# Kernel tuning notes

Hardware: AMD Instinct MI355X
Metric: run time of the kernel (lower is better)

The kernel has to match this reference:

```python
import jax, jax.numpy as jnp
import numpy as np

B, C, RES, WS, HEADS, GROUPS, MLP_DIM = 16, 256, 56, 7, 8, 16, 1024
HEAD_DIM = C // HEADS
N = WS * WS  # tokens per window


def _rel_index(ws):
    coords = np.stack(np.meshgrid(np.arange(ws), np.arange(ws), indexing='ij'), 0).reshape(2, -1)
    rel = (coords[:, :, None] - coords[:, None, :]).transpose(1, 2, 0) + ws - 1
    return jnp.asarray(rel[..., 0] * (2 * ws - 1) + rel[..., 1], jnp.int32)


def setup_inputs() -> dict:
    key = jax.random.key(0)
    ks = jax.random.split(key, 8)
    s = 0.02
    return {
        'x': jax.random.normal(ks[0], (B, C, RES, RES), jnp.float32),
        'qkv_w': jax.random.normal(ks[1], (3 * C, C), jnp.float32) * s,
        'qkv_b': jnp.zeros((3 * C,), jnp.float32),
        'logit_scale': jnp.full((HEADS,), np.log(10.0), jnp.float32),
        'bias_table': jax.random.normal(ks[2], ((2 * WS - 1) ** 2, HEADS), jnp.float32) * s,
        'rel_index': _rel_index(WS),
        'proj_w': jax.random.normal(ks[3], (C, C), jnp.float32) * s,
        'proj_b': jnp.zeros((C,), jnp.float32),
        'gn1_w': jnp.ones((C,), jnp.float32), 'gn1_b': jnp.zeros((C,), jnp.float32),
        'gn2_w': jnp.ones((C,), jnp.float32), 'gn2_b': jnp.zeros((C,), jnp.float32),
        'mlp_gn_w': jnp.ones((C,), jnp.float32), 'mlp_gn_b': jnp.zeros((C,), jnp.float32),
        'mlp_w1': jax.random.normal(ks[4], (MLP_DIM, C), jnp.float32) * s,
        'mlp_b1': jnp.zeros((MLP_DIM,), jnp.float32),
        'mlp_w2': jax.random.normal(ks[5], (C, MLP_DIM), jnp.float32) * s,
        'mlp_b2': jnp.zeros((C,), jnp.float32),
    }


def _group_norm(x, w, b, groups, eps=1e-5):
    bn, c, h, ww = x.shape
    xg = x.reshape(bn, groups, c // groups, h, ww)
    m = xg.mean((2, 3, 4), keepdims=True)
    v = xg.var((2, 3, 4), keepdims=True)
    xg = (xg - m) * jax.lax.rsqrt(v + eps)
    return xg.reshape(bn, c, h, ww) * w[None, :, None, None] + b[None, :, None, None]


def _window_cosine_attn(x, qkv_w, qkv_b, logit_scale, bias_table, rel_index, proj_w, proj_b):
    bn, c, hh, ww = x.shape
    nh, nw = hh // WS, ww // WS
    # partition into non-overlapping WSxWS windows -> [bn*nh*nw, N, C]
    xw = x.reshape(bn, c, nh, WS, nw, WS).transpose(0, 2, 4, 3, 5, 1).reshape(bn * nh * nw, N, c)
    qkv = xw @ qkv_w.T + qkv_b
    qkv = qkv.reshape(-1, N, 3, HEADS, HEAD_DIM).transpose(2, 0, 3, 1, 4)
    q, k, v = qkv[0], qkv[1], qkv[2]  # [Bw, heads, N, d]
    # cosine attention (Swin v2): l2-normalized q/k, learnable clamped logit scale
    qn = q / jnp.clip(jnp.linalg.norm(q, axis=-1, keepdims=True), 1e-12)
    kn = k / jnp.clip(jnp.linalg.norm(k, axis=-1, keepdims=True), 1e-12)
    scale = jnp.exp(jnp.minimum(logit_scale, jnp.log(100.0)))[None, :, None, None]
    attn = jnp.einsum('bhnd,bhmd->bhnm', qn, kn) * scale
    bias = bias_table[rel_index].transpose(2, 0, 1)  # [heads, N, N]
    attn = jax.nn.softmax(attn + bias[None], axis=-1)
    out = jnp.einsum('bhnm,bhmd->bhnd', attn, v)
    out = out.transpose(0, 2, 1, 3).reshape(-1, N, c) @ proj_w.T + proj_b
    # reverse window partition -> [bn, c, H, W]
    out = out.reshape(bn, nh, nw, WS, WS, c).transpose(0, 5, 1, 3, 2, 4).reshape(bn, c, hh, ww)
    return out


def reference(x, qkv_w, qkv_b, logit_scale, bias_table, rel_index, proj_w, proj_b,
              gn1_w, gn1_b, gn2_w, gn2_b, mlp_gn_w, mlp_gn_b, mlp_w1, mlp_b1, mlp_w2, mlp_b2):
    h = _window_cosine_attn(x, qkv_w, qkv_b, logit_scale, bias_table, rel_index, proj_w, proj_b)
    h = jax.nn.relu(_group_norm(x + h, gn1_w, gn1_b, GROUPS))
    # ConvMLP: GroupNorm -> 1x1 conv -> act -> 1x1 conv
    m = _group_norm(h, mlp_gn_w, mlp_gn_b, GROUPS)
    m = jax.nn.relu(jnp.einsum('bchw,ec->behw', m, mlp_w1) + mlp_b1[None, :, None, None])
    m = jnp.einsum('behw,ce->bchw', m, mlp_w2) + mlp_b2[None, :, None, None]
    z = jax.nn.relu(_group_norm(h + m, gn2_w, gn2_b, GROUPS))
    return z
```

## Files before the change

kernel.cpp:

```cpp
#include <hip/hip_runtime.h>
#include <hip/hip_bf16.h>

typedef unsigned short u16;
typedef u16 u16x8 __attribute__((ext_vector_type(8)));
typedef u16 u16x4 __attribute__((ext_vector_type(4)));
typedef __bf16 bf16x8 __attribute__((ext_vector_type(8)));
typedef float f32x4 __attribute__((ext_vector_type(4)));

#define B_      16
#define C_      256
#define RES_    56
#define HW_     3136
#define NTOK    49
#define HEADS_  8
#define HD_     32
#define GROUPS_ 16
#define MLPD    1024
#define M_TOT   50176

__device__ __forceinline__ float b2f(u16 u){
  unsigned int x = ((unsigned int)u) << 16;
  return __builtin_bit_cast(float, x);
}
__device__ __forceinline__ u16 f2b(float f){
  __hip_bfloat16 h = __float2bfloat16(f);
  return __builtin_bit_cast(u16, h);
}
__device__ __forceinline__ bool sniff_f32(const void* sniff){
  return ((const u16*)sniff)[0] != (u16)0x3F80;
}
__device__ __forceinline__ float ldf(const void* p, size_t i, bool f32){
  return f32 ? ((const float*)p)[i] : b2f(((const u16*)p)[i]);
}
__device__ __forceinline__ void load8(const void* p, size_t off, bool f32, float* v){
  if (f32){
    const float* s = (const float*)p + off;
    float4 a = *(const float4*)s, b = *(const float4*)(s + 4);
    v[0]=a.x; v[1]=a.y; v[2]=a.z; v[3]=a.w; v[4]=b.x; v[5]=b.y; v[6]=b.z; v[7]=b.w;
  } else {
    u16x8 u = *(const u16x8*)((const u16*)p + off);
    #pragma unroll
    for (int j=0;j<8;++j) v[j] = b2f(u[j]);
  }
}

__device__ __forceinline__ void gload16(const u16* g, u16* l){
  __builtin_amdgcn_global_load_lds(
      (const __attribute__((address_space(1))) unsigned int*)g,
      (__attribute__((address_space(3))) unsigned int*)l, 16, 0, 0);
}

__device__ __forceinline__ int tok_of(int base_hw, int i){
  int ic = i < 48 ? i : 48;
  int q = (ic*37) >> 8;
  return base_hw + q*RES_ + (ic - q*7);
}

enum { M_QKV=0, M_PROJ=1, M_MLP1=2, M_MLP2=3 };

template<int MODE>
__global__ __launch_bounds__(256)
void mgemm(const u16* __restrict__ A, const u16* __restrict__ Bseg,
           const void* __restrict__ bias, void* __restrict__ Cp,
           const void* __restrict__ resid, float2* __restrict__ partE,
           const void* __restrict__ sniff)
{
  constexpr int KK = (MODE==M_MLP2) ? 1024 : 256;
  constexpr bool STATS = (MODE==M_PROJ || MODE==M_MLP2);
  const int nx  = gridDim.x;
  const int bid = blockIdx.y * nx + blockIdx.x;
  const int cpx = (nx * gridDim.y) >> 3;
  const int swz = (bid & 7) * cpx + (bid >> 3);
  const int n0 = (swz % nx) * 128;
  const int m0 = (swz / nx) * 128;

  __shared__ alignas(16) u16 As[128*64];
  __shared__ alignas(16) u16 Bs[128*64];
  __shared__ float pS[4][2][4], pQ[4][2][4];
  const int tid  = threadIdx.x;
  const int lane = tid & 63, w = tid >> 6;
  const int wm = w >> 1, wn = w & 1;
  const int lr = lane & 15, lk = lane >> 4;

  const int grow = lane >> 3, gcolg = (lane & 7) ^ (lane >> 3);
  size_t aoff[4], boff[4];
  #pragma unroll
  for (int i=0;i<4;++i){
    const int row = w*32 + i*8 + grow;
    aoff[i] = (size_t)(m0 + row)*KK + gcolg*8;
    boff[i] = (size_t)(n0 + row)*KK + gcolg*8;
  }

  f32x4 acc[4][4];
  #pragma unroll
  for (int i=0;i<4;++i)
    #pragma unroll
    for (int j=0;j<4;++j) acc[i][j] = (f32x4){0.f,0.f,0.f,0.f};

  for (int k0 = 0; k0 < KK; k0 += 64){
    if (k0) __syncthreads();
    #pragma unroll
    for (int i=0;i<4;++i){
      gload16(A    + aoff[i] + k0, As + (w*4+i)*512);
      gload16(Bseg + boff[i] + k0, Bs + (w*4+i)*512);
    }
    __syncthreads();
    #pragma unroll
    for (int kh=0; kh<2; ++kh){
      bf16x8 af[4], bfr[4];
      #pragma unroll
      for (int mf=0;mf<4;++mf){
        int row = wm*64 + mf*16 + lr;
        int idx = (row*64 + (kh*4 + lk)*8) ^ ((row&7)*8);
        af[mf] = *(const bf16x8*)(As + idx);
      }
      #pragma unroll
      for (int nf=0;nf<4;++nf){
        int row = wn*64 + nf*16 + lr;
        int idx = (row*64 + (kh*4 + lk)*8) ^ ((row&7)*8);
        bfr[nf] = *(const bf16x8*)(Bs + idx);
      }
      #pragma unroll
      for (int mf=0;mf<4;++mf)
        #pragma unroll
        for (int nf=0;nf<4;++nf)
          acc[mf][nf] = __builtin_amdgcn_mfma_f32_16x16x32_bf16(af[mf], bfr[nf], acc[mf][nf], 0,0,0);
    }
  }

  const bool f32 = sniff_f32(sniff);
  float bv[4];
  #pragma unroll
  for (int nf=0;nf<4;++nf) bv[nf] = ldf(bias, (size_t)(n0 + wn*64 + nf*16 + lr), f32);

  const int b0 = m0 / HW_;
  const int splitB = (b0+1)*HW_;
  float sv[2][4] = {{0.f,0.f,0.f,0.f},{0.f,0.f,0.f,0.f}};
  float qv[2][4] = {{0.f,0.f,0.f,0.f},{0.f,0.f,0.f,0.f}};

  #pragma unroll
  for (int mf=0;mf<4;++mf){
    #pragma unroll
    for (int r=0;r<4;++r){
      const int row = m0 + wm*64 + mf*16 + lk*4 + r;
      #pragma unroll
      for (int nf=0;nf<4;++nf){
        const int col = n0 + wn*64 + nf*16 + lr;
        float v = acc[mf][nf][r] + bv[nf];
        if (MODE == M_QKV){
          ((u16*)Cp)[(size_t)row*768 + col] = f2b(v);
        } else if (MODE == M_MLP1){
          ((u16*)Cp)[(size_t)row*MLPD + col] = f2b(fmaxf(v, 0.f));
        } else {
          v += b2f(((const u16*)resid)[(size_t)row*C_ + col]);
          ((float*)Cp)[(size_t)row*C_ + col] = v;
          if constexpr (STATS){
            int slot = row >= splitB ? 1 : 0;
            sv[slot][nf] += v; qv[slot][nf] += v*v;
          }
        }
      }
    }
  }

  if constexpr (STATS){
    #pragma unroll
    for (int sl=0;sl<2;++sl)
      #pragma unroll
      for (int nf=0;nf<4;++nf){
        float s = sv[sl][nf], q = qv[sl][nf];
        #pragma unroll
        for (int m=1;m<64;m<<=1){ s += __shfl_xor(s,m); q += __shfl_xor(q,m); }
        if (lane == 0){ pS[w][sl][nf] = s; pQ[w][sl][nf] = q; }
      }
    __syncthreads();
    if (tid < 16){
      int slot = tid >> 3, gi = tid & 7, wn_ = gi >> 2, nf = gi & 3;
      float s = pS[wn_][slot][nf] + pS[2+wn_][slot][nf];
      float q = pQ[wn_][slot][nf] + pQ[2+wn_][slot][nf];
      partE[(((size_t)((m0>>7)*2 + (n0>>7)))*2 + slot)*8 + gi] = make_float2(s,q);
    }
  }
}

__global__ __launch_bounds__(256)
void xt_kernel(const void* __restrict__ x, u16* __restrict__ xbf,
               const void* __restrict__ sniff){
  const bool f32 = sniff_f32(sniff);
  const int hw0 = blockIdx.x*64, c0 = blockIdx.y*64, b = blockIdx.z;
  __shared__ float tile[64][65];
  const int t = threadIdx.x;
  {
    int r = t >> 2, p = t & 3;
    size_t src = ((size_t)(b*C_ + c0 + r))*HW_ + hw0 + p*16;
    float v[16];
    load8(x, src, f32, v);
    load8(x, src + 8, f32, v + 8);
    #pragma unroll
    for (int e=0;e<16;++e) tile[p*16+e][r] = v[e];
  }
  __syncthreads();
  {
    int r2 = t >> 2, p2 = t & 3;
    u16x8 o0, o1;
    #pragma unroll
    for (int e=0;e<8;++e){ o0[e] = f2b(tile[r2][p2*16+e]); o1[e] = f2b(tile[r2][p2*16+8+e]); }
    size_t dst = ((size_t)(b*HW_ + hw0 + r2))*C_ + c0 + p2*16;
    *(u16x8*)(xbf + dst)     = o0;
    *(u16x8*)(xbf + dst + 8) = o1;
  }
}

__global__ __launch_bounds__(256)
void wconv(const void* __restrict__ src, u16* __restrict__ dst, int n,
           const void* __restrict__ sniff){
  const bool f32 = sniff_f32(sniff);
  int i = (blockIdx.x*256 + threadIdx.x)*8;
  if (i >= n) return;
  float v[8];
  load8(src, (size_t)i, f32, v);
  u16x8 u;
  #pragma unroll
  for (int j=0;j<8;++j) u[j] = f2b(v[j]);
  *(u16x8*)(dst + i) = u;
}

__global__ __launch_bounds__(256)
void bias_pre(const void* __restrict__ bias_table, const int* __restrict__ rel_index,
              float* __restrict__ out, float* __restrict__ rmax,
              const void* __restrict__ sniff){
  const bool f32 = sniff_f32(sniff);
  int h = blockIdx.x;
  for (int idx = threadIdx.x; idx < NTOK*NTOK; idx += 256)
    out[h*NTOK*NTOK + idx] = ldf(bias_table, (size_t)rel_index[idx]*HEADS_ + h, f32);
  __syncthreads();
  for (int i = threadIdx.x; i < NTOK; i += 256){
    const float* row = out + (h*NTOK + i)*NTOK;
    float m = row[0];
    for (int j=1;j<NTOK;++j) m = fmaxf(m, row[j]);
    rmax[h*NTOK + i] = m;
  }
}

__global__ __launch_bounds__(256)
void attn_kernel(const u16* __restrict__ qkv, u16* __restrict__ attnout,
                 const void* __restrict__ logit_scale, const float* __restrict__ biasD,
                 const float* __restrict__ biasRM, const void* __restrict__ sniff)
{
  const bool f32 = sniff_f32(sniff);
  const int h = blockIdx.x & 7, w = blockIdx.x >> 3;
  const int b = w >> 6, wr = (w >> 3) & 7, wc = w & 7;
  const int tid = threadIdx.x;
  const int wv = tid >> 6, lane = tid & 63;
  const int lr = lane & 15, lg = lane >> 4;
  const int base_hw = (wr*7)*RES_ + wc*7;
  const size_t qbase = (size_t)b*HW_*768;

  __shared__ alignas(16) u16 Qn[64][40];
  __shared__ alignas(16) u16 Kn[64][40];
  __shared__ alignas(16) u16 Vt[32][72];
  __shared__ alignas(16) u16 Pl[64][72];

  const float scale = __expf(fminf(ldf(logit_scale, h, f32), 4.6051701860f));

  if (wv == 0){
    u16 vrow[32];
    if (lane < NTOK){
      const u16* src = qkv + qbase + (size_t)tok_of(base_hw, lane)*768 + 512 + h*HD_;
      u16x8 a0 = *(const u16x8*)(src), a1 = *(const u16x8*)(src+8);
      u16x8 a2 = *(const u16x8*)(src+16), a3 = *(const u16x8*)(src+24);
      #pragma unroll
      for (int e=0;e<8;++e){ vrow[e]=a0[e]; vrow[8+e]=a1[e]; vrow[16+e]=a2[e]; vrow[24+e]=a3[e]; }
    } else {
      #pragma unroll
      for (int e=0;e<32;++e) vrow[e] = 0;
    }
    #pragma unroll
    for (int d=0;d<32;++d) Vt[d][lane] = vrow[d];
  } else if (wv == 1 || wv == 2){
    float fv[32];
    if (lane < NTOK){
      const u16* src = qkv + qbase + (size_t)tok_of(base_hw, lane)*768
                     + (wv == 2 ? 0 : 256) + h*HD_;
      #pragma unroll
      for (int c8=0;c8<4;++c8){
        u16x8 u = *(const u16x8*)(src + c8*8);
        #pragma unroll
        for (int e=0;e<8;++e) fv[c8*8+e] = b2f(u[e]);
      }
    } else {
      #pragma unroll
      for (int e=0;e<32;++e) fv[e] = 0.f;
    }
    float ss = 0.f;
    #pragma unroll
    for (int d=0;d<32;++d) ss += fv[d]*fv[d];
    float inv = (wv == 2 ? scale : 1.f) / fmaxf(sqrtf(ss), 1e-12f);
    u16* dst = (wv == 2) ? &Qn[lane][0] : &Kn[lane][0];
    #pragma unroll
    for (int c8=0;c8<4;++c8){
      u16x8 u;
      #pragma unroll
      for (int e=0;e<8;++e) u[e] = f2b(fv[c8*8+e]*inv);
      *(u16x8*)(dst + c8*8) = u;
    }
  }
  __syncthreads();

  const int mt = wv;
  const int i0 = mt*16;

  bf16x8 af = *(const bf16x8*)&Qn[i0 + lr][lg*8];
  f32x4 s[4];
  #pragma unroll
  for (int nt=0;nt<4;++nt){
    bf16x8 bq = *(const bf16x8*)&Kn[nt*16 + lr][lg*8];
    f32x4 c;
    #pragma unroll
    for (int r=0;r<4;++r){
      int i = i0 + lg*4 + r; if (i > 48) i = 48;
      int j = nt*16 + lr;    if (j > 48) j = 48;
      c[r] = biasD[((size_t)h*NTOK + i)*NTOK + j];
    }
    s[nt] = __builtin_amdgcn_mfma_f32_16x16x32_bf16(af, bq, c, 0,0,0);
  }

  float isum[4];
  #pragma unroll
  for (int r=0;r<4;++r){
    const int i = i0 + lg*4 + r;
    const int ic = i > 48 ? 48 : i;
    const float m = scale + biasRM[h*NTOK + ic];
    float ps = 0.f;
    #pragma unroll
    for (int nt=0;nt<4;++nt){
      const int j = nt*16 + lr;
      float p = (j < NTOK) ? __expf(s[nt][r] - m) : 0.f;
      Pl[i][j] = f2b(p);
      ps += p;
    }
    ps += __shfl_xor(ps,1); ps += __shfl_xor(ps,2);
    ps += __shfl_xor(ps,4); ps += __shfl_xor(ps,8);
    isum[r] = 1.f / ps;
  }

  f32x4 o[2];
  o[0] = (f32x4){0.f,0.f,0.f,0.f};
  o[1] = (f32x4){0.f,0.f,0.f,0.f};
  #pragma unroll
  for (int kk=0;kk<2;++kk){
    bf16x8 pa = *(const bf16x8*)&Pl[i0 + lr][kk*32 + lg*8];
    #pragma unroll
    for (int nt=0;nt<2;++nt){
      bf16x8 pb = *(const bf16x8*)&Vt[nt*16 + lr][kk*32 + lg*8];
      o[nt] = __builtin_amdgcn_mfma_f32_16x16x32_bf16(pa, pb, o[nt], 0,0,0);
    }
  }

  #pragma unroll
  for (int r=0;r<4;++r){
    const int i = i0 + lg*4 + r;
    if (i < NTOK){
      size_t ob = ((size_t)(b*HW_) + tok_of(base_hw, i))*C_ + h*HD_;
      attnout[ob + lr]      = f2b(o[0][r] * isum[r]);
      attnout[ob + 16 + lr] = f2b(o[1][r] * isum[r]);
    }
  }
}

__global__ __launch_bounds__(256)
void statsE_fin(const float2* __restrict__ partE, float2* __restrict__ AB,
                const void* __restrict__ w, const void* __restrict__ bb,
                const void* __restrict__ sniff){
  const int b = blockIdx.x, t = threadIdx.x;
  const int g = t & 15, ch = t >> 4;
  const int ntI = g >> 3, gi = g & 7;
  float s = 0.f, q = 0.f;
  int mt0 = ch*25, mt1 = mt0 + 25 > 392 ? 392 : mt0 + 25;
  for (int mt = mt0; mt < mt1; ++mt){
    int b0 = (mt*128)/HW_;
    size_t base = ((size_t)(mt*2 + ntI))*16;
    if (b0 == b)    { float2 p = partE[base + gi];     s += p.x; q += p.y; }
    if (b0 + 1 == b){ float2 p = partE[base + 8 + gi]; s += p.x; q += p.y; }
  }
  __shared__ float Ls[256], Lq[256];
  Ls[t] = s; Lq[t] = q;
  __syncthreads();
  if (t < 16){
    float ss = 0.f, qq = 0.f;
    #pragma unroll
    for (int c=0;c<16;++c){ ss += Ls[c*16 + t]; qq += Lq[c*16 + t]; }
    float mean = ss * (1.f/50176.f);
    float var  = fmaxf(qq * (1.f/50176.f) - mean*mean, 0.f);
    float rsig = rsqrtf(var + 1e-5f);
    const bool f32 = sniff_f32(sniff);
    for (int e=0;e<16;++e){
      int k = t*16 + e;
      float a = rsig * ldf(w, k, f32);
      AB[b*256 + k] = make_float2(a, ldf(bb, k, f32) - mean*a);
    }
  }
}

__global__ __launch_bounds__(256)
void stats_fin2(const float2* __restrict__ part2, float2* __restrict__ AB,
                const void* __restrict__ w, const void* __restrict__ bb,
                const void* __restrict__ sniff){
  const int b = blockIdx.x, t = threadIdx.x;
  const int g = t & 15, ch = t >> 4;
  float s = 0.f, q = 0.f;
  int i0 = ch*25, i1 = i0 + 25 > 392 ? 392 : i0 + 25;
  for (int i = i0; i < i1; ++i){
    float2 p = part2[(size_t)(b*392 + i)*16 + g];
    s += p.x; q += p.y;
  }
  __shared__ float Ls[256], Lq[256];
  Ls[t] = s; Lq[t] = q;
  __syncthreads();
  if (t < 16){
    float ss = 0.f, qq = 0.f;
    #pragma unroll
    for (int c=0;c<16;++c){ ss += Ls[c*16 + t]; qq += Lq[c*16 + t]; }
    float mean = ss * (1.f/50176.f);
    float var  = fmaxf(qq * (1.f/50176.f) - mean*mean, 0.f);
    float rsig = rsqrtf(var + 1e-5f);
    const bool f32 = sniff_f32(sniff);
    for (int e=0;e<16;++e){
      int k = t*16 + e;
      float a = rsig * ldf(w, k, f32);
      AB[b*256 + k] = make_float2(a, ldf(bb, k, f32) - mean*a);
    }
  }
}

__global__ __launch_bounds__(256)
void gnrelu_kernel(const float* __restrict__ Y, const float2* __restrict__ AB1,
                   float2* __restrict__ part2, u16* __restrict__ Hb){
  size_t base = (size_t)blockIdx.x * 2048;
  int b = blockIdx.x / 392;
  int t = threadIdx.x;
  int off = t * 8;
  int c0 = off & 255;
  const float* src = Y + base + off;
  float4 a0 = *(const float4*)src, a1 = *(const float4*)(src+4);
  float tv[8] = {a0.x,a0.y,a0.z,a0.w,a1.x,a1.y,a1.z,a1.w};
  u16x8 u; float s=0.f, q=0.f;
  #pragma unroll
  for (int j=0;j<8;++j){
    float2 ab = AB1[b*256 + c0 + j];
    float o = fmaxf(tv[j]*ab.x + ab.y, 0.f);
    u[j] = f2b(o);
    s += o; q += o*o;
  }
  *(u16x8*)(Hb + base + off) = u;
  __shared__ float Ls[256], Lq[256];
  Ls[t] = s; Lq[t] = q;
  __syncthreads();
  if (t < 16){
    float ss=0.f, qq=0.f;
    #pragma unroll
    for (int j=0;j<16;++j){
      int idx = t*2 + (j&1) + (j>>1)*32;
      ss += Ls[idx]; qq += Lq[idx];
    }
    part2[(size_t)blockIdx.x*16 + t] = make_float2(ss,qq);
  }
}

__global__ __launch_bounds__(256)
void hnorm_kernel(const u16* __restrict__ Hb, const float2* __restrict__ AB,
                  u16* __restrict__ Hn){
  size_t base = (size_t)blockIdx.x * 2048;
  int b = blockIdx.x / 392;
  int off = threadIdx.x * 8;
  int c0 = off & 255;
  u16x8 uin = *(const u16x8*)(Hb + base + off);
  u16x8 u;
  #pragma unroll
  for (int j=0;j<8;++j){
    float2 ab = AB[b*256 + c0 + j];
    u[j] = f2b(b2f(uin[j])*ab.x + ab.y);
  }
  *(u16x8*)(Hn + base + off) = u;
}

__global__ __launch_bounds__(256)
void out_kernel(const float* __restrict__ T, const float2* __restrict__ AB2,
                void* __restrict__ outp, const void* __restrict__ sniff){
  const bool f32 = sniff_f32(sniff);
  int hw0 = blockIdx.x*64, c0 = blockIdx.y*64, b = blockIdx.z;
  __shared__ float tile[64][68];
  {
    int r = threadIdx.x >> 2, p = threadIdx.x & 3;
    const float* src = T + ((size_t)(b*HW_ + hw0 + r))*C_ + c0 + p*16;
    #pragma unroll
    for (int q4=0; q4<4; ++q4){
      float4 vv = *(const float4*)(src + q4*4);
      float tv[4] = {vv.x,vv.y,vv.z,vv.w};
      #pragma unroll
      for (int e=0;e<4;++e){
        int cl = p*16 + q4*4 + e;
        int c = c0 + cl;
        float2 ab = AB2[b*256 + c];
        tile[cl][r] = fmaxf(tv[e]*ab.x + ab.y, 0.f);
      }
    }
  }
  __syncthreads();
  {
    int r2 = threadIdx.x >> 2, p2 = threadIdx.x & 3;
    size_t ob = ((size_t)(b*C_ + c0 + r2))*HW_ + hw0 + p2*16;
    if (f32){
      float* op = (float*)outp;
      #pragma unroll
      for (int q4=0;q4<4;++q4){
        float4 vv = *(const float4*)&tile[r2][p2*16 + q4*4];
        *(float4*)(op + ob + q4*4) = vv;
      }
    } else {
      u16* op = (u16*)outp;
      u16x8 u0, u1;
      #pragma unroll
      for (int e=0;e<8;++e) u0[e] = f2b(tile[r2][p2*16 + e]);
      #pragma unroll
      for (int e=0;e<8;++e) u1[e] = f2b(tile[r2][p2*16 + 8 + e]);
      *(u16x8*)(op + ob)     = u0;
      *(u16x8*)(op + ob + 8) = u1;
    }
  }
}

__global__ void marker_kernel(u16* o){ o[threadIdx.x] = 0x4640; }

extern "C" void kernel_launch(void* const* d_in, const int* in_sizes, int n_in,
                              void* d_out, int out_size, void* d_ws, size_t ws_size,
                              hipStream_t stream)
{
  const void* x           = d_in[0];
  const void* qkv_w       = d_in[1];
  const void* qkv_b       = d_in[2];
  const void* logit_scale = d_in[3];
  const void* bias_table  = d_in[4];
  const int*  rel_index   = (const int*)d_in[5];
  const void* proj_w      = d_in[6];
  const void* proj_b      = d_in[7];
  const void* gn1_w       = d_in[8];
  const void* gn1_b       = d_in[9];
  const void* gn2_w       = d_in[10];
  const void* gn2_b       = d_in[11];
  const void* mgn_w       = d_in[12];
  const void* mgn_b       = d_in[13];
  const void* w1          = d_in[14];
  const void* b1          = d_in[15];
  const void* w2          = d_in[16];
  const void* b2          = d_in[17];

  char* ws = (char*)d_ws;
  const size_t o_qkv  = 0ull;
  const size_t o_attn = 77070336ull;
  const size_t o_Y    = 102760448ull;
  const size_t o_H    = 154140672ull;
  const size_t o_st   = 205520896ull;
  const size_t o_wbf  = 205527040ull;
  const size_t o_bd   = 207099904ull;
  const size_t o_brm  = 207176736ull;
  const size_t o_ab   = 207178304ull;
  const size_t o_ab1  = 207227456ull;
  const size_t o_ab2  = 207260224ull;
  const size_t o_p2   = 207292992ull;
  const size_t need   = 208095808ull;
  if (ws_size < need){
    marker_kernel<<<1, 256, 0, stream>>>((u16*)d_out);
    return;
  }

  u16*   qkvbuf  = (u16*)(ws + o_qkv);
  u16*   attnbuf = (u16*)(ws + o_attn);
  float* Y       = (float*)(ws + o_Y);
  u16*   Hb      = (u16*)(ws + o_H);
  u16*   xbf     = (u16*)(ws + o_H);
  u16*   Hn      = (u16*)(ws + o_Y);
  u16*   M1      = (u16*)(ws + o_qkv);
  float* T       = (float*)(ws + o_Y);
  u16*   wq      = (u16*)(ws + o_wbf);
  u16*   wp      = wq + 768*256;
  u16*   w1b     = wp + 256*256;
  u16*   w2b     = w1b + 1024*256;
  float* biasD   = (float*)(ws + o_bd);
  float* biasRM  = (float*)(ws + o_brm);
  float2* ABm    = (float2*)(ws + o_ab);
  float2* AB1    = (float2*)(ws + o_ab1);
  float2* AB2    = (float2*)(ws + o_ab2);
  float2* part2  = (float2*)(ws + o_p2);
  float2* partE  = (float2*)(ws + o_p2);
  const void* sniff = gn1_w;

  wconv        <<<  96, 256, 0, stream>>>(qkv_w,  wq,  768*256,  sniff);
  wconv        <<<  32, 256, 0, stream>>>(proj_w, wp,  256*256,  sniff);
  wconv        <<< 128, 256, 0, stream>>>(w1,     w1b, 1024*256, sniff);
  wconv        <<< 128, 256, 0, stream>>>(w2,     w2b, 256*1024, sniff);
  bias_pre     <<<   8, 256, 0, stream>>>(bias_table, rel_index, biasD, biasRM, sniff);
  xt_kernel    <<<dim3(49,4,16), 256, 0, stream>>>(x, xbf, sniff);

  mgemm<M_QKV ><<<dim3(6,392), 256, 0, stream>>>(xbf, wq, qkv_b, qkvbuf, nullptr, nullptr, sniff);
  attn_kernel  <<<8192, 256, 0, stream>>>(qkvbuf, attnbuf, logit_scale, biasD, biasRM, sniff);
  mgemm<M_PROJ><<<dim3(2,392), 256, 0, stream>>>(attnbuf, wp, proj_b, Y, xbf, partE, sniff);
  statsE_fin   <<<16, 256, 0, stream>>>(partE, AB1, gn1_w, gn1_b, sniff);
  gnrelu_kernel<<<6272, 256, 0, stream>>>(Y, AB1, part2, Hb);
  stats_fin2   <<<16, 256, 0, stream>>>(part2, ABm, mgn_w, mgn_b, sniff);
  hnorm_kernel <<<6272, 256, 0, stream>>>(Hb, ABm, Hn);
  mgemm<M_MLP1><<<dim3(8,392), 256, 0, stream>>>(Hn, w1b, b1, M1, nullptr, nullptr, sniff);
  mgemm<M_MLP2><<<dim3(2,392), 256, 0, stream>>>(M1, w2b, b2, T, Hb, partE, sniff);
  statsE_fin   <<<16, 256, 0, stream>>>(partE, AB2, gn2_w, gn2_b, sniff);
  out_kernel   <<<dim3(49,4,16), 256, 0, stream>>>(T, AB2, d_out, sniff);
}
```

Baseline: 313.1 us.

## Store projection and MLP2 outputs as bf16 and write per-wave stats directly

The PROJ and MLP2 GEMM epilogues now write their residual-added outputs as bf16 instead of fp32, which halves the intermediate traffic read back by the GroupNorm-ReLU and output kernels. The GEMM also drops its shared-memory stats reduction and barrier: each wave writes its partial sums straight to global memory, and the finalize kernel now sums the extra wave slots. The cost is lower precision on the pre-normalization activations, while the statistics are still accumulated in fp32.

```diff
diff --git a/kernel.cpp b/kernel.cpp
--- a/kernel.cpp
+++ b/kernel.cpp
@@ -76,7 +76,6 @@
 
   __shared__ alignas(16) u16 As[128*64];
   __shared__ alignas(16) u16 Bs[128*64];
-  __shared__ float pS[4][2][4], pQ[4][2][4];
   const int tid  = threadIdx.x;
   const int lane = tid & 63, w = tid >> 6;
   const int wm = w >> 1, wn = w & 1;
@@ -153,7 +152,7 @@
           ((u16*)Cp)[(size_t)row*MLPD + col] = f2b(fmaxf(v, 0.f));
         } else {
           v += b2f(((const u16*)resid)[(size_t)row*C_ + col]);
-          ((float*)Cp)[(size_t)row*C_ + col] = v;
+          ((u16*)Cp)[(size_t)row*C_ + col] = f2b(v);
           if constexpr (STATS){
             int slot = row >= splitB ? 1 : 0;
             sv[slot][nf] += v; qv[slot][nf] += v*v;
@@ -164,6 +163,7 @@
   }
 
   if constexpr (STATS){
+    const size_t tileId = (size_t)((m0>>7)*2 + (n0>>7));
     #pragma unroll
     for (int sl=0;sl<2;++sl)
       #pragma unroll
@@ -171,15 +171,9 @@
         float s = sv[sl][nf], q = qv[sl][nf];
         #pragma unroll
         for (int m=1;m<64;m<<=1){ s += __shfl_xor(s,m); q += __shfl_xor(q,m); }
-        if (lane == 0){ pS[w][sl][nf] = s; pQ[w][sl][nf] = q; }
+        if (lane == 0)
+          partE[(tileId*2 + sl)*16 + w*4 + nf] = make_float2(s,q);
       }
-    __syncthreads();
-    if (tid < 16){
-      int slot = tid >> 3, gi = tid & 7, wn_ = gi >> 2, nf = gi & 3;
-      float s = pS[wn_][slot][nf] + pS[2+wn_][slot][nf];
-      float q = pQ[wn_][slot][nf] + pQ[2+wn_][slot][nf];
-      partE[(((size_t)((m0>>7)*2 + (n0>>7)))*2 + slot)*8 + gi] = make_float2(s,q);
-    }
   }
 }
 
@@ -374,14 +368,22 @@
                 const void* __restrict__ sniff){
   const int b = blockIdx.x, t = threadIdx.x;
   const int g = t & 15, ch = t >> 4;
-  const int ntI = g >> 3, gi = g & 7;
+  const int ntI = g >> 3, wn_ = (g >> 2) & 1, nf = g & 3;
   float s = 0.f, q = 0.f;
   int mt0 = ch*25, mt1 = mt0 + 25 > 392 ? 392 : mt0 + 25;
   for (int mt = mt0; mt < mt1; ++mt){
     int b0 = (mt*128)/HW_;
-    size_t base = ((size_t)(mt*2 + ntI))*16;
-    if (b0 == b)    { float2 p = partE[base + gi];     s += p.x; q += p.y; }
-    if (b0 + 1 == b){ float2 p = partE[base + 8 + gi]; s += p.x; q += p.y; }
+    size_t base = ((size_t)(mt*2 + ntI))*32;
+    if (b0 == b){
+      float2 p0 = partE[base + wn_*4 + nf];
+      float2 p1 = partE[base + 8 + wn_*4 + nf];
+      s += p0.x + p1.x; q += p0.y + p1.y;
+    }
+    if (b0 + 1 == b){
+      float2 p0 = partE[base + 16 + wn_*4 + nf];
+      float2 p1 = partE[base + 24 + wn_*4 + nf];
+      s += p0.x + p1.x; q += p0.y + p1.y;
+    }
   }
   __shared__ float Ls[256], Lq[256];
   Ls[t] = s; Lq[t] = q;
@@ -434,21 +436,19 @@
 }
 
 __global__ __launch_bounds__(256)
-void gnrelu_kernel(const float* __restrict__ Y, const float2* __restrict__ AB1,
+void gnrelu_kernel(const u16* __restrict__ Yb, const float2* __restrict__ AB1,
                    float2* __restrict__ part2, u16* __restrict__ Hb){
   size_t base = (size_t)blockIdx.x * 2048;
   int b = blockIdx.x / 392;
   int t = threadIdx.x;
   int off = t * 8;
   int c0 = off & 255;
-  const float* src = Y + base + off;
-  float4 a0 = *(const float4*)src, a1 = *(const float4*)(src+4);
-  float tv[8] = {a0.x,a0.y,a0.z,a0.w,a1.x,a1.y,a1.z,a1.w};
+  u16x8 uin = *(const u16x8*)(Yb + base + off);
   u16x8 u; float s=0.f, q=0.f;
   #pragma unroll
   for (int j=0;j<8;++j){
     float2 ab = AB1[b*256 + c0 + j];
-    float o = fmaxf(tv[j]*ab.x + ab.y, 0.f);
+    float o = fmaxf(b2f(uin[j])*ab.x + ab.y, 0.f);
     u[j] = f2b(o);
     s += o; q += o*o;
   }
@@ -485,25 +485,23 @@
 }
 
 __global__ __launch_bounds__(256)
-void out_kernel(const float* __restrict__ T, const float2* __restrict__ AB2,
+void out_kernel(const u16* __restrict__ T, const float2* __restrict__ AB2,
                 void* __restrict__ outp, const void* __restrict__ sniff){
   const bool f32 = sniff_f32(sniff);
   int hw0 = blockIdx.x*64, c0 = blockIdx.y*64, b = blockIdx.z;
   __shared__ float tile[64][68];
   {
     int r = threadIdx.x >> 2, p = threadIdx.x & 3;
-    const float* src = T + ((size_t)(b*HW_ + hw0 + r))*C_ + c0 + p*16;
-    #pragma unroll
-    for (int q4=0; q4<4; ++q4){
-      float4 vv = *(const float4*)(src + q4*4);
-      float tv[4] = {vv.x,vv.y,vv.z,vv.w};
-      #pragma unroll
-      for (int e=0;e<4;++e){
-        int cl = p*16 + q4*4 + e;
-        int c = c0 + cl;
-        float2 ab = AB2[b*256 + c];
-        tile[cl][r] = fmaxf(tv[e]*ab.x + ab.y, 0.f);
-      }
+    const u16* src = T + ((size_t)(b*HW_ + hw0 + r))*C_ + c0 + p*16;
+    u16x8 v0 = *(const u16x8*)(src);
+    u16x8 v1 = *(const u16x8*)(src + 8);
+    #pragma unroll
+    for (int e=0;e<16;++e){
+      int cl = p*16 + e;
+      int c = c0 + cl;
+      float2 ab = AB2[b*256 + c];
+      float tv = b2f(e < 8 ? v0[e] : v1[e-8]);
+      tile[cl][r] = fmaxf(tv*ab.x + ab.y, 0.f);
     }
   }
   __syncthreads();
@@ -560,7 +558,6 @@
   const size_t o_attn = 77070336ull;
   const size_t o_Y    = 102760448ull;
   const size_t o_H    = 154140672ull;
-  const size_t o_st   = 205520896ull;
   const size_t o_wbf  = 205527040ull;
   const size_t o_bd   = 207099904ull;
   const size_t o_brm  = 207176736ull;
@@ -576,12 +573,12 @@
 
   u16*   qkvbuf  = (u16*)(ws + o_qkv);
   u16*   attnbuf = (u16*)(ws + o_attn);
-  float* Y       = (float*)(ws + o_Y);
+  u16*   Yb      = (u16*)(ws + o_Y);
   u16*   Hb      = (u16*)(ws + o_H);
   u16*   xbf     = (u16*)(ws + o_H);
   u16*   Hn      = (u16*)(ws + o_Y);
   u16*   M1      = (u16*)(ws + o_qkv);
-  float* T       = (float*)(ws + o_Y);
+  u16*   T       = (u16*)(ws + o_Y);
   u16*   wq      = (u16*)(ws + o_wbf);
   u16*   wp      = wq + 768*256;
   u16*   w1b     = wp + 256*256;
@@ -604,9 +601,9 @@
 
   mgemm<M_QKV ><<<dim3(6,392), 256, 0, stream>>>(xbf, wq, qkv_b, qkvbuf, nullptr, nullptr, sniff);
   attn_kernel  <<<8192, 256, 0, stream>>>(qkvbuf, attnbuf, logit_scale, biasD, biasRM, sniff);
-  mgemm<M_PROJ><<<dim3(2,392), 256, 0, stream>>>(attnbuf, wp, proj_b, Y, xbf, partE, sniff);
+  mgemm<M_PROJ><<<dim3(2,392), 256, 0, stream>>>(attnbuf, wp, proj_b, Yb, xbf, partE, sniff);
   statsE_fin   <<<16, 256, 0, stream>>>(partE, AB1, gn1_w, gn1_b, sniff);
-  gnrelu_kernel<<<6272, 256, 0, stream>>>(Y, AB1, part2, Hb);
+  gnrelu_kernel<<<6272, 256, 0, stream>>>(Yb, AB1, part2, Hb);
   stats_fin2   <<<16, 256, 0, stream>>>(part2, ABm, mgn_w, mgn_b, sniff);
   hnorm_kernel <<<6272, 256, 0, stream>>>(Hb, ABm, Hn);
   mgemm<M_MLP1><<<dim3(8,392), 256, 0, stream>>>(Hn, w1b, b1, M1, nullptr, nullptr, sniff);
```

New measurement: 314.4 us. About the same (+0.4%).
